# Kernel tuning notes

Hardware: AMD Instinct MI355X
Metric: run time of the kernel (lower is better)

Reference implementation:

```python
import jax, jax.numpy as jnp
import numpy as np
from jax.ops import segment_sum

N_GRAPHS, N_PER = 100, 1000
N = N_GRAPHS * N_PER
DEG = 32
E = N * DEG
RATIO = 0.8
K = int(np.ceil(RATIO * N_PER))  # 800, equal-size graphs -> fixed k
F_IN, F_MID, F_OUT = 128, 16, 256


def setup_inputs() -> dict:
    key = jax.random.key(0)
    ks = jax.random.split(key, 10)
    x = jax.random.normal(ks[0], (N, F_IN), dtype=jnp.float32)
    # intra-graph random edges
    epg = E // N_GRAPHS
    src_l = jax.random.randint(ks[1], (N_GRAPHS, epg), 0, N_PER)
    dst_l = jax.random.randint(ks[2], (N_GRAPHS, epg), 0, N_PER)
    offs = (jnp.arange(N_GRAPHS) * N_PER)[:, None]
    edge_index = jnp.stack([(src_l + offs).reshape(-1), (dst_l + offs).reshape(-1)]).astype(jnp.int32)
    batch = jnp.repeat(jnp.arange(N_GRAPHS, dtype=jnp.int32), N_PER)
    s = lambda fan: 1.0 / np.sqrt(fan)
    W1 = jax.random.normal(ks[3], (F_IN, F_MID), dtype=jnp.float32) * s(F_IN)
    b1 = jnp.zeros((F_MID,), dtype=jnp.float32)
    w_rel = jax.random.normal(ks[4], (F_MID, 1), dtype=jnp.float32) * s(F_MID)
    b_rel = jnp.zeros((1,), dtype=jnp.float32)
    w_root = jax.random.normal(ks[5], (F_MID, 1), dtype=jnp.float32) * s(F_MID)
    W2 = jax.random.normal(ks[6], (F_MID, F_OUT), dtype=jnp.float32) * s(F_MID)
    b2 = jnp.zeros((F_OUT,), dtype=jnp.float32)
    return {"x": x, "edge_index": edge_index, "batch": batch,
            "W1": W1, "b1": b1, "w_rel": w_rel, "b_rel": b_rel,
            "w_root": w_root, "W2": W2, "b2": b2}


def _gcn(x, src, dst, W, b, self_w, ew, n):
    # GCNConv with self-loops: D^{-1/2}(A+I)D^{-1/2} X W + b; masked variant
    deg = segment_sum(ew, dst, num_segments=n) + self_w
    dis = jnp.where(deg > 0, jax.lax.rsqrt(deg), 0.0)
    xw = x @ W
    coef = ew * dis[src] * dis[dst]                       # [E]
    agg = segment_sum(xw[src] * coef[:, None], dst, num_segments=n)
    agg = agg + xw * (self_w * dis * dis)[:, None]        # self-loop term
    return agg + b


def reference(x, edge_index, batch, W1, b1, w_rel, b_rel, w_root, W2, b2):
    src, dst = edge_index[0], edge_index[1]
    ones_n = jnp.ones((N,), dtype=x.dtype)
    ones_e = jnp.ones((src.shape[0],), dtype=x.dtype)
    # conv1 + relu
    h = jax.nn.relu(_gcn(x, src, dst, W1, b1, ones_n, ones_e, N))
    # SAGPooling score: GraphConv(16,1) -> tanh
    agg = segment_sum(h[src], dst, num_segments=N)
    score = jnp.tanh((agg @ w_rel + h @ w_root + b_rel)[:, 0])  # [N]
    # per-graph top-k (equal graph sizes -> fixed K), expressed as node mask
    sc2 = score.reshape(N_GRAPHS, N_PER)
    _, idx = jax.lax.top_k(sc2, K)
    mask = jnp.zeros((N_GRAPHS, N_PER), dtype=x.dtype)
    mask = mask.at[jnp.arange(N_GRAPHS)[:, None], idx].set(1.0).reshape(-1)  # [N]
    h = h * (score * mask)[:, None]                       # x[perm] * score[perm]
    em = mask[src] * mask[dst]                            # filter_adj as edge mask
    # conv2 + relu on surviving nodes only
    h2 = jax.nn.relu(_gcn(h, src, dst, W2, b2, mask, em, N)) * mask[:, None]
    # global mean pool over surviving nodes per graph
    sums = segment_sum(h2, batch, num_segments=N_GRAPHS)
    cnt = segment_sum(mask, batch, num_segments=N_GRAPHS)
    return sums / cnt[:, None]
```

## Files before the change

kernel.cpp:

```cpp
#include <hip/hip_runtime.h>
#include <math.h>

#define N_NODES 100000
#define NG 100
#define N_PER 1000
#define N_EDGES 3200000
#define EPG 32000
#define EPG4 8000
#define EPGP 35008
#define K_TOP 800
#define F_IN 128
#define F_MID 16
#define F_OUT 256
#define SENT 1000

typedef __attribute__((ext_vector_type(8))) short short8;
typedef __attribute__((ext_vector_type(4))) float floatx4;

__device__ __forceinline__ unsigned short f2bf(float x) {
    union { float f; unsigned int u; } c; c.f = x;
    unsigned int u = c.u;
    u = u + 0x7FFF + ((u >> 16) & 1);
    return (unsigned short)(u >> 16);
}
__device__ __forceinline__ void add4(float4& a, const float4 b) {
    a.x += b.x; a.y += b.y; a.z += b.z; a.w += b.w;
}
__device__ __forceinline__ int fidx4(int s, int l) {
    return s * 16 + ((4 * (l + ((s >> 1) & 3))) & 15);
}
__device__ __forceinline__ unsigned int fkey(float f) {
    unsigned int u = __float_as_uint(f);
    return (u & 0x80000000u) ? ~u : (u | 0x80000000u);
}

__global__ __launch_bounds__(1024) void k_front(const float* __restrict__ x,
    const float* __restrict__ W1, const int* __restrict__ ei,
    unsigned short* __restrict__ csr, int* __restrict__ cntG, int* __restrict__ rsG,
    float* __restrict__ dis1G, float* __restrict__ xw1)
{
    int b = blockIdx.x, t = threadIdx.x;
    if (b < NG) {
        __shared__ int cnts[N_PER];
        __shared__ int cur[N_PER];
        __shared__ int rs[N_PER];
        __shared__ int scan[1024];
        int g = b, ebase = g * EPG, nbase = g * N_PER;
        const int4* dst4 = (const int4*)(ei + N_EDGES + ebase);
        const int4* src4 = (const int4*)(ei + ebase);
        int4 dreg[8], sreg[8];
        int ni = 0;
        for (int i = t; i < EPG4; i += 1024) { dreg[ni] = dst4[i]; sreg[ni] = src4[i]; ni++; }
        if (t < N_PER) { cnts[t] = 0; cur[t] = 0; }
        __syncthreads();
        for (int i = 0; i < ni; i++) {
            atomicAdd(&cnts[dreg[i].x - nbase], 1);
            atomicAdd(&cnts[dreg[i].y - nbase], 1);
            atomicAdd(&cnts[dreg[i].z - nbase], 1);
            atomicAdd(&cnts[dreg[i].w - nbase], 1);
        }
        __syncthreads();
        int c = (t < N_PER) ? cnts[t] : 0;
        int c4 = (c + 3) & ~3;
        scan[t] = c4;
        __syncthreads();
        for (int dd = 1; dd < 1024; dd <<= 1) {
            int v = (t >= dd) ? scan[t - dd] : 0;
            __syncthreads();
            scan[t] += v;
            __syncthreads();
        }
        int exc = scan[t] - c4;
        unsigned short* cg = csr + (size_t)g * EPGP;
        if (t < N_PER) {
            rs[t] = exc; rsG[nbase + t] = exc; cntG[nbase + t] = c;
            dis1G[nbase + t] = rsqrtf((float)c + 1.0f);
            for (int q = c; q < c4; q++) cg[exc + q] = (unsigned short)SENT;
        }
        __syncthreads();
        for (int i = 0; i < ni; i++) {
            int dl, p;
            dl = dreg[i].x - nbase; p = rs[dl] + atomicAdd(&cur[dl], 1); cg[p] = (unsigned short)(sreg[i].x - nbase);
            dl = dreg[i].y - nbase; p = rs[dl] + atomicAdd(&cur[dl], 1); cg[p] = (unsigned short)(sreg[i].y - nbase);
            dl = dreg[i].z - nbase; p = rs[dl] + atomicAdd(&cur[dl], 1); cg[p] = (unsigned short)(sreg[i].z - nbase);
            dl = dreg[i].w - nbase; p = rs[dl] + atomicAdd(&cur[dl], 1); cg[p] = (unsigned short)(sreg[i].w - nbase);
        }
    } else {
        __shared__ float xs[64 * 132];
        __shared__ float wsm[F_IN * F_MID];
        long tile = b - NG;
        long n0 = tile * 64;
        int nmax = (int)((N_NODES - n0 < 64) ? (N_NODES - n0) : 64);
        const float* xp = x + n0 * F_IN;
        for (int i = t; i < nmax * F_IN; i += 1024) {
            int n = i >> 7, k = i & 127;
            xs[n * 132 + k] = xp[i];
        }
        for (int i = t; i < F_IN * F_MID; i += 1024) wsm[i] = W1[i];
        __syncthreads();
        int node = t >> 4, j = t & 15;
        if (node < nmax) {
            const float* xr = xs + node * 132;
            float acc = 0.f;
#pragma unroll 16
            for (int k = 0; k < F_IN; k++) acc += xr[k] * wsm[k * F_MID + j];
            xw1[(n0 + node) * F_MID + j] = acc;
        }
    }
}

__global__ __launch_bounds__(1024) void k_mega(const unsigned short* __restrict__ csr,
    const int* __restrict__ cntG, const int* __restrict__ rsG,
    const float* __restrict__ dis1G, const float* __restrict__ xw1,
    const float* __restrict__ b1, const float* __restrict__ w_rel,
    const float* __restrict__ b_rel, const float* __restrict__ w_root,
    const float* __restrict__ W2, const float* __restrict__ b2,
    float* __restrict__ out)
{
    __shared__ __align__(16) float feat[(N_PER + 1) * F_MID];
    __shared__ __align__(16) unsigned short fbf[N_PER * F_MID];
    __shared__ __align__(16) unsigned short w2t[F_OUT * F_MID];
    __shared__ float sc[N_PER];
    __shared__ float msk[N_PER + 1];
    __shared__ float wsrc[N_PER + 1];
    __shared__ float hw[N_PER + 1];
    __shared__ float hro[N_PER];
    __shared__ float dis2a[N_PER];
    __shared__ float dis1l[N_PER];
    __shared__ int cntl[N_PER];
    __shared__ int rsl[N_PER];
    __shared__ int hist[1024];
    __shared__ float partial[F_OUT];
    __shared__ int sh_b1, sh_r1, sh_b2, sh_r2, sh_len, sh_cntgt;
    __shared__ float sh_thr;

    int t = threadIdx.x, g = blockIdx.x;
    int nbase = g * N_PER;
    const unsigned short* cg = csr + (size_t)g * EPGP;
    int grp = t >> 2, l = t & 3;

    if (t < N_PER) { cntl[t] = cntG[nbase + t]; rsl[t] = rsG[nbase + t]; dis1l[t] = dis1G[nbase + t]; }
    if (t == 0) { sh_cntgt = 0; sh_len = 0; }
    for (int i = t; i < F_OUT * F_MID; i += 1024) {
        int f = i >> 4, jj = i & 15;
        w2t[i] = f2bf(W2[jj * F_OUT + f]);
    }
    __syncthreads();

    {
        const float4* xsrc = (const float4*)(xw1 + (size_t)nbase * F_MID);
        for (int i = t; i < N_PER * 4; i += 1024) {
            int n = i >> 2, q = i & 3;
            float4 v = xsrc[i];
            float d = dis1l[n];
            v.x *= d; v.y *= d; v.z *= d; v.w *= d;
            *(float4*)(feat + fidx4(n, q)) = v;
        }
        if (t < 4) { float4 z = {0.f, 0.f, 0.f, 0.f}; *(float4*)(feat + fidx4(SENT, t)) = z; }
    }
    __syncthreads();

    float4 b14 = *(const float4*)(b1 + 4 * l);
    float4 wr4 = *(const float4*)(w_rel + 4 * l);
    float4 wo4 = *(const float4*)(w_root + 4 * l);
    float brel = b_rel[0];

    float4 hreg[4];
#pragma unroll
    for (int rr = 0; rr < 4; rr++) {
        int n = grp + 256 * rr;
        if (n < N_PER) {
            int c4 = (cntl[n] + 3) & ~3;
            const unsigned short* cp = cg + rsl[n];
            float4 a0 = {0,0,0,0}, a1 = a0, a2 = a0, a3 = a0;
            for (int k = 0; k < c4; k += 4) {
                uint2 wv = *(const uint2*)(cp + k);
                int s0 = wv.x & 0xFFFF, s1 = wv.x >> 16, s2 = wv.y & 0xFFFF, s3 = wv.y >> 16;
                add4(a0, *(const float4*)(feat + fidx4(s0, l)));
                add4(a1, *(const float4*)(feat + fidx4(s1, l)));
                add4(a2, *(const float4*)(feat + fidx4(s2, l)));
                add4(a3, *(const float4*)(feat + fidx4(s3, l)));
            }
            add4(a0, a1); add4(a2, a3); add4(a0, a2);
            float4 sf = *(const float4*)(feat + fidx4(n, l));
            float di = dis1l[n];
            float4 hv;
            hv.x = fmaxf(fmaf(di, a0.x + sf.x, b14.x), 0.f);
            hv.y = fmaxf(fmaf(di, a0.y + sf.y, b14.y), 0.f);
            hv.z = fmaxf(fmaf(di, a0.z + sf.z, b14.z), 0.f);
            hv.w = fmaxf(fmaf(di, a0.w + sf.w, b14.w), 0.f);
            hreg[rr] = hv;
        }
    }
    __syncthreads();
#pragma unroll
    for (int rr = 0; rr < 4; rr++) {
        int n = grp + 256 * rr;
        if (n < N_PER) *(float4*)(feat + fidx4(n, l)) = hreg[rr];
    }
    __syncthreads();

#pragma unroll
    for (int rr = 0; rr < 4; rr++) {
        int n = grp + 256 * rr;
        if (n < N_PER) {
            float4 hv = *(const float4*)(feat + fidx4(n, l));
            float p1 = hv.x * wr4.x + hv.y * wr4.y + hv.z * wr4.z + hv.w * wr4.w;
            float p2 = hv.x * wo4.x + hv.y * wo4.y + hv.z * wo4.z + hv.w * wo4.w;
            p1 += __shfl_xor(p1, 1); p1 += __shfl_xor(p1, 2);
            p2 += __shfl_xor(p2, 1); p2 += __shfl_xor(p2, 2);
            if (l == 0) { hw[n] = p1; hro[n] = p2; }
        }
    }
    if (t == 0) hw[SENT] = 0.f;
    __syncthreads();

#pragma unroll
    for (int rr = 0; rr < 4; rr++) {
        int n = grp + 256 * rr;
        if (n < N_PER) {
            int c4 = (cntl[n] + 3) & ~3;
            const unsigned short* cp = cg + rsl[n];
            float sm = 0.f;
            for (int k = 0; k < c4; k += 4) {
                uint2 wv = *(const uint2*)(cp + k);
                int s = (l == 0) ? (int)(wv.x & 0xFFFF) : (l == 1) ? (int)(wv.x >> 16)
                      : (l == 2) ? (int)(wv.y & 0xFFFF) : (int)(wv.y >> 16);
                sm += hw[s];
            }
            sm += __shfl_xor(sm, 1); sm += __shfl_xor(sm, 2);
            if (l == 0) sc[n] = tanhf(sm + hro[n] + brel);
        }
    }
    __syncthreads();

    unsigned int mykey = (t < N_PER) ? fkey(sc[t]) : 0u;
    hist[t] = 0;
    __syncthreads();
    if (t < N_PER) atomicAdd(&hist[mykey >> 22], 1);
    __syncthreads();
    {
        int v0 = hist[t]; __syncthreads();
        hist[1023 - t] = v0; __syncthreads();
        for (int dd = 1; dd < 1024; dd <<= 1) {
            int v = (t >= dd) ? hist[t - dd] : 0;
            __syncthreads(); hist[t] += v; __syncthreads();
        }
        int Sb = hist[1023 - t];
        int Snext = (t == 1023) ? 0 : hist[1022 - t];
        if (Sb >= K_TOP && Snext < K_TOP) { sh_b1 = t; sh_r1 = K_TOP - Snext; }
    }
    __syncthreads();
    int b1v = sh_b1, r1 = sh_r1;
    hist[t] = 0;
    __syncthreads();
    if (t < N_PER && (int)(mykey >> 22) == b1v) atomicAdd(&hist[(mykey >> 12) & 1023], 1);
    __syncthreads();
    {
        int v0 = hist[t]; __syncthreads();
        hist[1023 - t] = v0; __syncthreads();
        for (int dd = 1; dd < 1024; dd <<= 1) {
            int v = (t >= dd) ? hist[t - dd] : 0;
            __syncthreads(); hist[t] += v; __syncthreads();
        }
        int Sb = hist[1023 - t];
        int Snext = (t == 1023) ? 0 : hist[1022 - t];
        if (Sb >= r1 && Snext < r1) { sh_b2 = t; sh_r2 = r1 - Snext; }
    }
    __syncthreads();
    unsigned int pref = ((unsigned int)b1v << 10) | (unsigned int)sh_b2;
    int r2 = sh_r2;
    __syncthreads();
    if (t < N_PER && (mykey >> 12) == pref) { int p = atomicAdd(&sh_len, 1); hist[p] = (int)mykey; }
    __syncthreads();
    {
        int L = sh_len;
        if (t < L) {
            unsigned int k0 = (unsigned int)hist[t];
            int gcnt = 0, ecnt = 0;
            for (int q2 = 0; q2 < L; q2++) {
                unsigned int kq = (unsigned int)hist[q2];
                gcnt += (kq > k0); ecnt += (kq == k0);
            }
            if (gcnt < r2 && r2 <= gcnt + ecnt)
                sh_thr = __uint_as_float((k0 & 0x80000000u) ? (k0 & 0x7FFFFFFFu) : ~k0);
        }
    }
    __syncthreads();
    float thr = sh_thr;

    {
        bool pred = (t < N_PER) && (sc[t] > thr);
        unsigned long long bal = __ballot(pred);
        if ((t & 63) == 0) atomicAdd(&sh_cntgt, (int)__popcll(bal));
    }
    __syncthreads();
    {
        int need = K_TOP - sh_cntgt;
        if (t < N_PER) {
            float v = sc[t];
            float mm;
            if (v > thr) mm = 1.f;
            else if (v < thr) mm = 0.f;
            else {
                int r = 0;
                for (int q2 = 0; q2 < t; q2++) if (sc[q2] == thr) r++;
                mm = (r < need) ? 1.f : 0.f;
            }
            msk[t] = mm;
        }
        if (t == 0) { msk[SENT] = 0.f; wsrc[SENT] = 0.f; }
    }
    __syncthreads();

#pragma unroll
    for (int rr = 0; rr < 4; rr++) {
        int n = grp + 256 * rr;
        if (n < N_PER) {
            int c4 = (cntl[n] + 3) & ~3;
            const unsigned short* cp = cg + rsl[n];
            float sm = 0.f;
            for (int k = 0; k < c4; k += 4) {
                uint2 wv = *(const uint2*)(cp + k);
                int s = (l == 0) ? (int)(wv.x & 0xFFFF) : (l == 1) ? (int)(wv.x >> 16)
                      : (l == 2) ? (int)(wv.y & 0xFFFF) : (int)(wv.y >> 16);
                sm += msk[s];
            }
            sm += __shfl_xor(sm, 1); sm += __shfl_xor(sm, 2);
            if (l == 0) {
                float d2 = msk[n] * (sm + 1.f);
                float di = (d2 > 0.f) ? rsqrtf(d2) : 0.f;
                dis2a[n] = di;
                wsrc[n] = sc[n] * msk[n] * di;
            }
        }
    }
    __syncthreads();

    for (int i = t; i < N_PER * 4; i += 1024) {
        int n = i >> 2, q = i & 3;
        float w = wsrc[n];
        float4* p = (float4*)(feat + fidx4(n, q));
        float4 v = *p;
        v.x *= w; v.y *= w; v.z *= w; v.w *= w;
        *p = v;
    }
    __syncthreads();

    float4 preg[4];
#pragma unroll
    for (int rr = 0; rr < 4; rr++) {
        int n = grp + 256 * rr;
        if (n < N_PER) {
            float di = dis2a[n];
            float4 pv = {0,0,0,0};
            if (di != 0.f) {
                int c4 = (cntl[n] + 3) & ~3;
                const unsigned short* cp = cg + rsl[n];
                float4 a0 = {0,0,0,0}, a1 = a0, a2 = a0, a3 = a0;
                for (int k = 0; k < c4; k += 4) {
                    uint2 wv = *(const uint2*)(cp + k);
                    int s0 = wv.x & 0xFFFF, s1 = wv.x >> 16, s2 = wv.y & 0xFFFF, s3 = wv.y >> 16;
                    add4(a0, *(const float4*)(feat + fidx4(s0, l)));
                    add4(a1, *(const float4*)(feat + fidx4(s1, l)));
                    add4(a2, *(const float4*)(feat + fidx4(s2, l)));
                    add4(a3, *(const float4*)(feat + fidx4(s3, l)));
                }
                add4(a0, a1); add4(a2, a3); add4(a0, a2);
                float4 sf = *(const float4*)(feat + fidx4(n, l));
                pv.x = di * (a0.x + sf.x);
                pv.y = di * (a0.y + sf.y);
                pv.z = di * (a0.z + sf.z);
                pv.w = di * (a0.w + sf.w);
            }
            preg[rr] = pv;
        }
    }
    __syncthreads();
#pragma unroll
    for (int rr = 0; rr < 4; rr++) {
        int n = grp + 256 * rr;
        if (n < N_PER) *(float4*)(feat + fidx4(n, l)) = preg[rr];
    }
    __syncthreads();

    for (int i = t; i < N_PER * 8; i += 1024) {
        int n = i >> 3, cp2 = (i & 7) * 2;
        int phys = n * 16 + ((cp2 + 4 * ((n >> 1) & 3)) & 15);
        float2 v = *(const float2*)(feat + phys);
        unsigned int pk = (unsigned int)f2bf(v.x) | ((unsigned int)f2bf(v.y) << 16);
        ((unsigned int*)fbf)[i] = pk;
    }
    __syncthreads();

    {
        int wave = t >> 6, lane = t & 63;
        int q = lane >> 4, fl = lane & 15;
        int half = wave >> 3, wcol = wave & 7;
        int c0 = 32 * wcol + fl, c1 = c0 + 16;
        float b2f0 = b2[c0], b2f1 = b2[c1];
        short8 bfrag0 = {0,0,0,0,0,0,0,0}, bfrag1 = bfrag0;
        if (q < 2) {
            bfrag0 = *(const short8*)(w2t + c0 * F_MID + q * 8);
            bfrag1 = *(const short8*)(w2t + c1 * F_MID + q * 8);
        }
        floatx4 zero = {0.f, 0.f, 0.f, 0.f};
        float acc0 = 0.f, acc1 = 0.f;
        int t0 = half ? 32 : 0, t1 = half ? 63 : 32;
        for (int tile = t0; tile < t1; tile++) {
            short8 afrag = {0,0,0,0,0,0,0,0};
            int na = tile * 16 + fl;
            if (q < 2 && na < N_PER)
                afrag = *(const short8*)(fbf + na * F_MID + q * 8);
            floatx4 d0 = __builtin_amdgcn_mfma_f32_16x16x32_bf16(afrag, bfrag0, zero, 0, 0, 0);
            floatx4 d1 = __builtin_amdgcn_mfma_f32_16x16x32_bf16(afrag, bfrag1, zero, 0, 0, 0);
#pragma unroll
            for (int r = 0; r < 4; r++) {
                int nd = tile * 16 + q * 4 + r;
                if (nd < N_PER) {
                    float m = msk[nd];
                    acc0 += m * fmaxf(d0[r] + b2f0, 0.f);
                    acc1 += m * fmaxf(d1[r] + b2f1, 0.f);
                }
            }
        }
        acc0 += __shfl_xor(acc0, 16); acc0 += __shfl_xor(acc0, 32);
        acc1 += __shfl_xor(acc1, 16); acc1 += __shfl_xor(acc1, 32);
        if (half == 0 && lane < 16) { partial[c0] = acc0; partial[c1] = acc1; }
        __syncthreads();
        if (half == 1 && lane < 16) {
            out[g * F_OUT + c0] = (partial[c0] + acc0) * (1.0f / (float)K_TOP);
            out[g * F_OUT + c1] = (partial[c1] + acc1) * (1.0f / (float)K_TOP);
        }
    }
}

extern "C" void kernel_launch(void* const* d_in, const int* in_sizes, int n_in,
                              void* d_out, int out_size, void* d_ws, size_t ws_size,
                              hipStream_t stream) {
    const float* x      = (const float*)d_in[0];
    const int*   ei     = (const int*)d_in[1];
    const float* W1     = (const float*)d_in[3];
    const float* b1     = (const float*)d_in[4];
    const float* w_rel  = (const float*)d_in[5];
    const float* b_rel  = (const float*)d_in[6];
    const float* w_root = (const float*)d_in[7];
    const float* W2     = (const float*)d_in[8];
    const float* b2     = (const float*)d_in[9];
    float* out = (float*)d_out;

    char* ws = (char*)d_ws;
    size_t o = 0;
    unsigned short* csr = (unsigned short*)(ws + o); o += (size_t)NG * EPGP * sizeof(unsigned short);
    int*   cntG  = (int*)(ws + o);   o += (size_t)N_NODES * sizeof(int);
    int*   rsG   = (int*)(ws + o);   o += (size_t)N_NODES * sizeof(int);
    float* dis1G = (float*)(ws + o); o += (size_t)N_NODES * sizeof(float);
    float* xw1   = (float*)(ws + o); o += (size_t)N_NODES * F_MID * sizeof(float);

    int gemm_blocks = (N_NODES + 63) / 64;
    k_front<<<NG + gemm_blocks, 1024, 0, stream>>>(x, W1, ei, csr, cntG, rsG, dis1G, xw1);
    k_mega<<<NG, 1024, 0, stream>>>(csr, cntG, rsG, dis1G, xw1,
                                    b1, w_rel, b_rel, w_root, W2, b2, out);
}
```

Measured before the change: 240.7 us.

## Use split-bf16 MFMA for first GEMM, pad CSR to 8, simplify top-k selection

Replaces the scalar x@W1 GEMM with a three-term split-bf16 MFMA (hi*hi + lo*hi + hi*lo) over 256-row tiles, and merges shared memory across the two roles of the front kernel. CSR rows are padded to multiples of 8 so the gathers load eight indices at a time into eight accumulators. The two-level radix top-k becomes one histogram level with wave-shuffle scans plus direct candidate ranking, and tie ranking uses bitmasks instead of a linear scan. Costs include more sentinel padding and memory, a single-level selection that may leave a large candidate bucket to rank, and slightly different GEMM rounding.

Result: no change. 241.8 us (+0.4%).

```diff
diff --git a/kernel.cpp b/kernel.cpp
--- a/kernel.cpp
+++ b/kernel.cpp
@@ -7,12 +7,14 @@
 #define N_EDGES 3200000
 #define EPG 32000
 #define EPG4 8000
-#define EPGP 35008
+#define EPGP 39008
 #define K_TOP 800
 #define F_IN 128
 #define F_MID 16
 #define F_OUT 256
 #define SENT 1000
+#define GEMM_ROWS 256
+#define GEMM_BLOCKS ((N_NODES + GEMM_ROWS - 1) / GEMM_ROWS)
 
 typedef __attribute__((ext_vector_type(8))) short short8;
 typedef __attribute__((ext_vector_type(4))) float floatx4;
@@ -23,6 +25,9 @@
     u = u + 0x7FFF + ((u >> 16) & 1);
     return (unsigned short)(u >> 16);
 }
+__device__ __forceinline__ float bf2f(unsigned short h) {
+    return __uint_as_float(((unsigned int)h) << 16);
+}
 __device__ __forceinline__ void add4(float4& a, const float4 b) {
     a.x += b.x; a.y += b.y; a.z += b.z; a.w += b.w;
 }
@@ -33,36 +38,38 @@
     unsigned int u = __float_as_uint(f);
     return (u & 0x80000000u) ? ~u : (u | 0x80000000u);
 }
+__device__ __forceinline__ float unfkey(unsigned int k) {
+    return __uint_as_float((k & 0x80000000u) ? (k & 0x7FFFFFFFu) : ~k);
+}
 
 __global__ __launch_bounds__(1024) void k_front(const float* __restrict__ x,
     const float* __restrict__ W1, const int* __restrict__ ei,
-    unsigned short* __restrict__ csr, int* __restrict__ cntG, int* __restrict__ rsG,
+    unsigned short* __restrict__ csr, int* __restrict__ cnt8G, int* __restrict__ rsG,
     float* __restrict__ dis1G, float* __restrict__ xw1)
 {
+    __shared__ __align__(16) char smem[16640];
     int b = blockIdx.x, t = threadIdx.x;
     if (b < NG) {
-        __shared__ int cnts[N_PER];
-        __shared__ int cur[N_PER];
-        __shared__ int rs[N_PER];
-        __shared__ int scan[1024];
+        int* cnts = (int*)smem;
+        int* cur  = (int*)(smem + 4000);
+        int* rs   = (int*)(smem + 8000);
+        int* scan = (int*)(smem + 12000);
         int g = b, ebase = g * EPG, nbase = g * N_PER;
         const int4* dst4 = (const int4*)(ei + N_EDGES + ebase);
         const int4* src4 = (const int4*)(ei + ebase);
-        int4 dreg[8], sreg[8];
-        int ni = 0;
-        for (int i = t; i < EPG4; i += 1024) { dreg[ni] = dst4[i]; sreg[ni] = src4[i]; ni++; }
         if (t < N_PER) { cnts[t] = 0; cur[t] = 0; }
         __syncthreads();
-        for (int i = 0; i < ni; i++) {
-            atomicAdd(&cnts[dreg[i].x - nbase], 1);
-            atomicAdd(&cnts[dreg[i].y - nbase], 1);
-            atomicAdd(&cnts[dreg[i].z - nbase], 1);
-            atomicAdd(&cnts[dreg[i].w - nbase], 1);
+        for (int i = t; i < EPG4; i += 1024) {
+            int4 d = dst4[i];
+            atomicAdd(&cnts[d.x - nbase], 1);
+            atomicAdd(&cnts[d.y - nbase], 1);
+            atomicAdd(&cnts[d.z - nbase], 1);
+            atomicAdd(&cnts[d.w - nbase], 1);
         }
         __syncthreads();
         int c = (t < N_PER) ? cnts[t] : 0;
-        int c4 = (c + 3) & ~3;
-        scan[t] = c4;
+        int c8 = (c + 7) & ~7;
+        scan[t] = c8;
         __syncthreads();
         for (int dd = 1; dd < 1024; dd <<= 1) {
             int v = (t >= dd) ? scan[t - dd] : 0;
@@ -70,47 +77,72 @@
             scan[t] += v;
             __syncthreads();
         }
-        int exc = scan[t] - c4;
+        int exc = scan[t] - c8;
         unsigned short* cg = csr + (size_t)g * EPGP;
         if (t < N_PER) {
-            rs[t] = exc; rsG[nbase + t] = exc; cntG[nbase + t] = c;
+            rs[t] = exc; rsG[nbase + t] = exc; cnt8G[nbase + t] = c8;
             dis1G[nbase + t] = rsqrtf((float)c + 1.0f);
-            for (int q = c; q < c4; q++) cg[exc + q] = (unsigned short)SENT;
-        }
-        __syncthreads();
-        for (int i = 0; i < ni; i++) {
+            for (int q = c; q < c8; q++) cg[exc + q] = (unsigned short)SENT;
+        }
+        __syncthreads();
+        for (int i = t; i < EPG4; i += 1024) {
+            int4 s4 = src4[i]; int4 d4 = dst4[i];
             int dl, p;
-            dl = dreg[i].x - nbase; p = rs[dl] + atomicAdd(&cur[dl], 1); cg[p] = (unsigned short)(sreg[i].x - nbase);
-            dl = dreg[i].y - nbase; p = rs[dl] + atomicAdd(&cur[dl], 1); cg[p] = (unsigned short)(sreg[i].y - nbase);
-            dl = dreg[i].z - nbase; p = rs[dl] + atomicAdd(&cur[dl], 1); cg[p] = (unsigned short)(sreg[i].z - nbase);
-            dl = dreg[i].w - nbase; p = rs[dl] + atomicAdd(&cur[dl], 1); cg[p] = (unsigned short)(sreg[i].w - nbase);
+            dl = d4.x - nbase; p = rs[dl] + atomicAdd(&cur[dl], 1); cg[p] = (unsigned short)(s4.x - nbase);
+            dl = d4.y - nbase; p = rs[dl] + atomicAdd(&cur[dl], 1); cg[p] = (unsigned short)(s4.y - nbase);
+            dl = d4.z - nbase; p = rs[dl] + atomicAdd(&cur[dl], 1); cg[p] = (unsigned short)(s4.z - nbase);
+            dl = d4.w - nbase; p = rs[dl] + atomicAdd(&cur[dl], 1); cg[p] = (unsigned short)(s4.w - nbase);
         }
     } else {
-        __shared__ float xs[64 * 132];
-        __shared__ float wsm[F_IN * F_MID];
-        long tile = b - NG;
-        long n0 = tile * 64;
-        int nmax = (int)((N_NODES - n0 < 64) ? (N_NODES - n0) : 64);
-        const float* xp = x + n0 * F_IN;
-        for (int i = t; i < nmax * F_IN; i += 1024) {
-            int n = i >> 7, k = i & 127;
-            xs[n * 132 + k] = xp[i];
-        }
-        for (int i = t; i < F_IN * F_MID; i += 1024) wsm[i] = W1[i];
-        __syncthreads();
-        int node = t >> 4, j = t & 15;
-        if (node < nmax) {
-            const float* xr = xs + node * 132;
-            float acc = 0.f;
-#pragma unroll 16
-            for (int k = 0; k < F_IN; k++) acc += xr[k] * wsm[k * F_MID + j];
-            xw1[(n0 + node) * F_MID + j] = acc;
+        unsigned short* bTh = (unsigned short*)smem;
+        unsigned short* bTl = (unsigned short*)(smem + 4096);
+        for (int i = t; i < F_IN * F_MID; i += 1024) {
+            int k = i >> 4, n = i & 15;
+            float w = W1[i];
+            unsigned short hh = f2bf(w);
+            bTh[n * 128 + k] = hh;
+            bTl[n * 128 + k] = f2bf(w - bf2f(hh));
+        }
+        __syncthreads();
+        int wave = t >> 6, lane = t & 63;
+        int m = lane & 15, q = lane >> 4;
+        long rbase = (long)(b - NG) * GEMM_ROWS + wave * 16;
+        long arow = rbase + m;
+        const float* xr = x + ((arow < N_NODES) ? arow : (N_NODES - 1)) * F_IN;
+        short8 ah[4], al[4], bh[4], bl[4];
+#pragma unroll
+        for (int c = 0; c < 4; c++) {
+            float4 v0 = *(const float4*)(xr + 32 * c + 8 * q);
+            float4 v1 = *(const float4*)(xr + 32 * c + 8 * q + 4);
+            float vv[8] = {v0.x, v0.y, v0.z, v0.w, v1.x, v1.y, v1.z, v1.w};
+            short8 h8, l8;
+#pragma unroll
+            for (int i = 0; i < 8; i++) {
+                unsigned short hh = f2bf(vv[i]);
+                h8[i] = (short)hh;
+                l8[i] = (short)f2bf(vv[i] - bf2f(hh));
+            }
+            ah[c] = h8; al[c] = l8;
+            bh[c] = *(const short8*)(bTh + m * 128 + 32 * c + 8 * q);
+            bl[c] = *(const short8*)(bTl + m * 128 + 32 * c + 8 * q);
+        }
+        floatx4 acc = {0.f, 0.f, 0.f, 0.f};
+#pragma unroll
+        for (int c = 0; c < 4; c++) {
+            acc = __builtin_amdgcn_mfma_f32_16x16x32_bf16(ah[c], bh[c], acc, 0, 0, 0);
+            acc = __builtin_amdgcn_mfma_f32_16x16x32_bf16(al[c], bh[c], acc, 0, 0, 0);
+            acc = __builtin_amdgcn_mfma_f32_16x16x32_bf16(ah[c], bl[c], acc, 0, 0, 0);
+        }
+#pragma unroll
+        for (int r = 0; r < 4; r++) {
+            long orow = rbase + q * 4 + r;
+            if (orow < N_NODES) xw1[orow * F_MID + m] = acc[r];
         }
     }
 }
 
 __global__ __launch_bounds__(1024) void k_mega(const unsigned short* __restrict__ csr,
-    const int* __restrict__ cntG, const int* __restrict__ rsG,
+    const int* __restrict__ cnt8G, const int* __restrict__ rsG,
     const float* __restrict__ dis1G, const float* __restrict__ xw1,
     const float* __restrict__ b1, const float* __restrict__ w_rel,
     const float* __restrict__ b_rel, const float* __restrict__ w_root,
@@ -127,20 +159,24 @@
     __shared__ float hro[N_PER];
     __shared__ float dis2a[N_PER];
     __shared__ float dis1l[N_PER];
-    __shared__ int cntl[N_PER];
+    __shared__ int cnt8l[N_PER];
     __shared__ int rsl[N_PER];
     __shared__ int hist[1024];
     __shared__ float partial[F_OUT];
-    __shared__ int sh_b1, sh_r1, sh_b2, sh_r2, sh_len, sh_cntgt;
+    __shared__ int wtot[16], wexc[16];
+    __shared__ unsigned int tiebits[32];
+    __shared__ int sh_b1, sh_r1, sh_len, sh_cntgt;
     __shared__ float sh_thr;
 
     int t = threadIdx.x, g = blockIdx.x;
     int nbase = g * N_PER;
     const unsigned short* cg = csr + (size_t)g * EPGP;
     int grp = t >> 2, l = t & 3;
-
-    if (t < N_PER) { cntl[t] = cntG[nbase + t]; rsl[t] = rsG[nbase + t]; dis1l[t] = dis1G[nbase + t]; }
+    int lane = t & 63, wid = t >> 6;
+
+    if (t < N_PER) { cnt8l[t] = cnt8G[nbase + t]; rsl[t] = rsG[nbase + t]; dis1l[t] = dis1G[nbase + t]; }
     if (t == 0) { sh_cntgt = 0; sh_len = 0; }
+    if (t < 32) tiebits[t] = 0;
     for (int i = t; i < F_OUT * F_MID; i += 1024) {
         int f = i >> 4, jj = i & 15;
         w2t[i] = f2bf(W2[jj * F_OUT + f]);
@@ -170,25 +206,29 @@
     for (int rr = 0; rr < 4; rr++) {
         int n = grp + 256 * rr;
         if (n < N_PER) {
-            int c4 = (cntl[n] + 3) & ~3;
+            int c8 = cnt8l[n];
             const unsigned short* cp = cg + rsl[n];
-            float4 a0 = {0,0,0,0}, a1 = a0, a2 = a0, a3 = a0;
-            for (int k = 0; k < c4; k += 4) {
-                uint2 wv = *(const uint2*)(cp + k);
-                int s0 = wv.x & 0xFFFF, s1 = wv.x >> 16, s2 = wv.y & 0xFFFF, s3 = wv.y >> 16;
-                add4(a0, *(const float4*)(feat + fidx4(s0, l)));
-                add4(a1, *(const float4*)(feat + fidx4(s1, l)));
-                add4(a2, *(const float4*)(feat + fidx4(s2, l)));
-                add4(a3, *(const float4*)(feat + fidx4(s3, l)));
-            }
-            add4(a0, a1); add4(a2, a3); add4(a0, a2);
+            float4 A0 = {0,0,0,0}, A1 = A0, A2 = A0, A3 = A0, A4 = A0, A5 = A0, A6 = A0, A7 = A0;
+            for (int k = 0; k < c8; k += 8) {
+                uint4 wv = *(const uint4*)(cp + k);
+                add4(A0, *(const float4*)(feat + fidx4((int)(wv.x & 0xFFFF), l)));
+                add4(A1, *(const float4*)(feat + fidx4((int)(wv.x >> 16), l)));
+                add4(A2, *(const float4*)(feat + fidx4((int)(wv.y & 0xFFFF), l)));
+                add4(A3, *(const float4*)(feat + fidx4((int)(wv.y >> 16), l)));
+                add4(A4, *(const float4*)(feat + fidx4((int)(wv.z & 0xFFFF), l)));
+                add4(A5, *(const float4*)(feat + fidx4((int)(wv.z >> 16), l)));
+                add4(A6, *(const float4*)(feat + fidx4((int)(wv.w & 0xFFFF), l)));
+                add4(A7, *(const float4*)(feat + fidx4((int)(wv.w >> 16), l)));
+            }
+            add4(A0, A1); add4(A2, A3); add4(A4, A5); add4(A6, A7);
+            add4(A0, A2); add4(A4, A6); add4(A0, A4);
             float4 sf = *(const float4*)(feat + fidx4(n, l));
             float di = dis1l[n];
             float4 hv;
-            hv.x = fmaxf(fmaf(di, a0.x + sf.x, b14.x), 0.f);
-            hv.y = fmaxf(fmaf(di, a0.y + sf.y, b14.y), 0.f);
-            hv.z = fmaxf(fmaf(di, a0.z + sf.z, b14.z), 0.f);
-            hv.w = fmaxf(fmaf(di, a0.w + sf.w, b14.w), 0.f);
+            hv.x = fmaxf(fmaf(di, A0.x + sf.x, b14.x), 0.f);
+            hv.y = fmaxf(fmaf(di, A0.y + sf.y, b14.y), 0.f);
+            hv.z = fmaxf(fmaf(di, A0.z + sf.z, b14.z), 0.f);
+            hv.w = fmaxf(fmaf(di, A0.w + sf.w, b14.w), 0.f);
             hreg[rr] = hv;
         }
     }
@@ -219,62 +259,57 @@
     for (int rr = 0; rr < 4; rr++) {
         int n = grp + 256 * rr;
         if (n < N_PER) {
-            int c4 = (cntl[n] + 3) & ~3;
+            int c8 = cnt8l[n];
             const unsigned short* cp = cg + rsl[n];
-            float sm = 0.f;
-            for (int k = 0; k < c4; k += 4) {
-                uint2 wv = *(const uint2*)(cp + k);
-                int s = (l == 0) ? (int)(wv.x & 0xFFFF) : (l == 1) ? (int)(wv.x >> 16)
-                      : (l == 2) ? (int)(wv.y & 0xFFFF) : (int)(wv.y >> 16);
-                sm += hw[s];
-            }
+            float s0 = 0.f, s1 = 0.f;
+            for (int k = 0; k < c8; k += 8) {
+                uint4 wv = *(const uint4*)(cp + k);
+                int sa = (l == 0) ? (int)(wv.x & 0xFFFF) : (l == 1) ? (int)(wv.x >> 16)
+                       : (l == 2) ? (int)(wv.y & 0xFFFF) : (int)(wv.y >> 16);
+                int sb = (l == 0) ? (int)(wv.z & 0xFFFF) : (l == 1) ? (int)(wv.z >> 16)
+                       : (l == 2) ? (int)(wv.w & 0xFFFF) : (int)(wv.w >> 16);
+                s0 += hw[sa]; s1 += hw[sb];
+            }
+            float sm = s0 + s1;
             sm += __shfl_xor(sm, 1); sm += __shfl_xor(sm, 2);
             if (l == 0) sc[n] = tanhf(sm + hro[n] + brel);
         }
     }
     __syncthreads();
 
-    unsigned int mykey = (t < N_PER) ? fkey(sc[t]) : 0u;
+    unsigned int mykey = 0; int myb = -1;
+    if (t < N_PER) { mykey = fkey(sc[t]); myb = (int)(mykey >> 22); }
     hist[t] = 0;
     __syncthreads();
-    if (t < N_PER) atomicAdd(&hist[mykey >> 22], 1);
+    if (t < N_PER) atomicAdd(&hist[myb], 1);
     __syncthreads();
     {
-        int v0 = hist[t]; __syncthreads();
-        hist[1023 - t] = v0; __syncthreads();
-        for (int dd = 1; dd < 1024; dd <<= 1) {
-            int v = (t >= dd) ? hist[t - dd] : 0;
-            __syncthreads(); hist[t] += v; __syncthreads();
-        }
-        int Sb = hist[1023 - t];
-        int Snext = (t == 1023) ? 0 : hist[1022 - t];
-        if (Sb >= K_TOP && Snext < K_TOP) { sh_b1 = t; sh_r1 = K_TOP - Snext; }
-    }
-    __syncthreads();
-    int b1v = sh_b1, r1 = sh_r1;
-    hist[t] = 0;
-    __syncthreads();
-    if (t < N_PER && (int)(mykey >> 22) == b1v) atomicAdd(&hist[(mykey >> 12) & 1023], 1);
+        int cntb = hist[t];
+        int v = cntb;
+        for (int off = 1; off < 64; off <<= 1) {
+            int u = __shfl_down(v, off, 64);
+            if (lane + off < 64) v += u;
+        }
+        if (lane == 0) wtot[wid] = v;
+        __syncthreads();
+        if (wid == 0) {
+            int wv2 = (lane < 16) ? wtot[lane] : 0;
+            int sv = wv2;
+            for (int off = 1; off < 16; off <<= 1) {
+                int u = __shfl_down(sv, off, 64);
+                if (lane + off < 64) sv += u;
+            }
+            if (lane < 16) wexc[lane] = sv - wv2;
+        }
+        __syncthreads();
+        int S = v + wexc[wid];
+        if (S >= K_TOP && S - cntb < K_TOP) { sh_b1 = t; sh_r1 = K_TOP - (S - cntb); }
+    }
+    __syncthreads();
+    if (t < N_PER && myb == sh_b1) { int p = atomicAdd(&sh_len, 1); hist[p] = (int)mykey; }
     __syncthreads();
     {
-        int v0 = hist[t]; __syncthreads();
-        hist[1023 - t] = v0; __syncthreads();
-        for (int dd = 1; dd < 1024; dd <<= 1) {
-            int v = (t >= dd) ? hist[t - dd] : 0;
-            __syncthreads(); hist[t] += v; __syncthreads();
-        }
-        int Sb = hist[1023 - t];
-        int Snext = (t == 1023) ? 0 : hist[1022 - t];
-        if (Sb >= r1 && Snext < r1) { sh_b2 = t; sh_r2 = r1 - Snext; }
-    }
-    __syncthreads();
-    unsigned int pref = ((unsigned int)b1v << 10) | (unsigned int)sh_b2;
-    int r2 = sh_r2;
-    __syncthreads();
-    if (t < N_PER && (mykey >> 12) == pref) { int p = atomicAdd(&sh_len, 1); hist[p] = (int)mykey; }
-    __syncthreads();
-    {
-        int L = sh_len;
+        int L = sh_len, r1 = sh_r1;
         if (t < L) {
             unsigned int k0 = (unsigned int)hist[t];
             int gcnt = 0, ecnt = 0;
@@ -282,8 +317,7 @@
                 unsigned int kq = (unsigned int)hist[q2];
                 gcnt += (kq > k0); ecnt += (kq == k0);
             }
-            if (gcnt < r2 && r2 <= gcnt + ecnt)
-                sh_thr = __uint_as_float((k0 & 0x80000000u) ? (k0 & 0x7FFFFFFFu) : ~k0);
+            if (gcnt < r1 && r1 <= gcnt + ecnt) sh_thr = unfkey(k0);
         }
     }
     __syncthreads();
@@ -291,11 +325,11 @@
 
     {
         bool pred = (t < N_PER) && (sc[t] > thr);
+        bool tied = (t < N_PER) && (sc[t] == thr);
         unsigned long long bal = __ballot(pred);
         if ((t & 63) == 0) atomicAdd(&sh_cntgt, (int)__popcll(bal));
-    }
-    __syncthreads();
-    {
+        if (tied) atomicOr(&tiebits[t >> 5], 1u << (t & 31));
+        __syncthreads();
         int need = K_TOP - sh_cntgt;
         if (t < N_PER) {
             float v = sc[t];
@@ -303,9 +337,10 @@
             if (v > thr) mm = 1.f;
             else if (v < thr) mm = 0.f;
             else {
-                int r = 0;
-                for (int q2 = 0; q2 < t; q2++) if (sc[q2] == thr) r++;
-                mm = (r < need) ? 1.f : 0.f;
+                int w = t >> 5;
+                int rank = __popc(tiebits[w] & ((1u << (t & 31)) - 1u));
+                for (int ww = 0; ww < w; ww++) rank += __popc(tiebits[ww]);
+                mm = (rank < need) ? 1.f : 0.f;
             }
             msk[t] = mm;
         }
@@ -317,15 +352,18 @@
     for (int rr = 0; rr < 4; rr++) {
         int n = grp + 256 * rr;
         if (n < N_PER) {
-            int c4 = (cntl[n] + 3) & ~3;
+            int c8 = cnt8l[n];
             const unsigned short* cp = cg + rsl[n];
-            float sm = 0.f;
-            for (int k = 0; k < c4; k += 4) {
-                uint2 wv = *(const uint2*)(cp + k);
-                int s = (l == 0) ? (int)(wv.x & 0xFFFF) : (l == 1) ? (int)(wv.x >> 16)
-                      : (l == 2) ? (int)(wv.y & 0xFFFF) : (int)(wv.y >> 16);
-                sm += msk[s];
-            }
+            float s0 = 0.f, s1 = 0.f;
+            for (int k = 0; k < c8; k += 8) {
+                uint4 wv = *(const uint4*)(cp + k);
+                int sa = (l == 0) ? (int)(wv.x & 0xFFFF) : (l == 1) ? (int)(wv.x >> 16)
+                       : (l == 2) ? (int)(wv.y & 0xFFFF) : (int)(wv.y >> 16);
+                int sb = (l == 0) ? (int)(wv.z & 0xFFFF) : (l == 1) ? (int)(wv.z >> 16)
+                       : (l == 2) ? (int)(wv.w & 0xFFFF) : (int)(wv.w >> 16);
+                s0 += msk[sa]; s1 += msk[sb];
+            }
+            float sm = s0 + s1;
             sm += __shfl_xor(sm, 1); sm += __shfl_xor(sm, 2);
             if (l == 0) {
                 float d2 = msk[n] * (sm + 1.f);
@@ -355,23 +393,27 @@
             float di = dis2a[n];
             float4 pv = {0,0,0,0};
             if (di != 0.f) {
-                int c4 = (cntl[n] + 3) & ~3;
+                int c8 = cnt8l[n];
                 const unsigned short* cp = cg + rsl[n];
-                float4 a0 = {0,0,0,0}, a1 = a0, a2 = a0, a3 = a0;
-                for (int k = 0; k < c4; k += 4) {
-                    uint2 wv = *(const uint2*)(cp + k);
-                    int s0 = wv.x & 0xFFFF, s1 = wv.x >> 16, s2 = wv.y & 0xFFFF, s3 = wv.y >> 16;
-                    add4(a0, *(const float4*)(feat + fidx4(s0, l)));
-                    add4(a1, *(const float4*)(feat + fidx4(s1, l)));
-                    add4(a2, *(const float4*)(feat + fidx4(s2, l)));
-                    add4(a3, *(const float4*)(feat + fidx4(s3, l)));
+                float4 A0 = {0,0,0,0}, A1 = A0, A2 = A0, A3 = A0, A4 = A0, A5 = A0, A6 = A0, A7 = A0;
+                for (int k = 0; k < c8; k += 8) {
+                    uint4 wv = *(const uint4*)(cp + k);
+                    add4(A0, *(const float4*)(feat + fidx4((int)(wv.x & 0xFFFF), l)));
+                    add4(A1, *(const float4*)(feat + fidx4((int)(wv.x >> 16), l)));
+                    add4(A2, *(const float4*)(feat + fidx4((int)(wv.y & 0xFFFF), l)));
+                    add4(A3, *(const float4*)(feat + fidx4((int)(wv.y >> 16), l)));
+                    add4(A4, *(const float4*)(feat + fidx4((int)(wv.z & 0xFFFF), l)));
+                    add4(A5, *(const float4*)(feat + fidx4((int)(wv.z >> 16), l)));
+                    add4(A6, *(const float4*)(feat + fidx4((int)(wv.w & 0xFFFF), l)));
+                    add4(A7, *(const float4*)(feat + fidx4((int)(wv.w >> 16), l)));
                 }
-                add4(a0, a1); add4(a2, a3); add4(a0, a2);
+                add4(A0, A1); add4(A2, A3); add4(A4, A5); add4(A6, A7);
+                add4(A0, A2); add4(A4, A6); add4(A0, A4);
                 float4 sf = *(const float4*)(feat + fidx4(n, l));
-                pv.x = di * (a0.x + sf.x);
-                pv.y = di * (a0.y + sf.y);
-                pv.z = di * (a0.z + sf.z);
-                pv.w = di * (a0.w + sf.w);
+                pv.x = di * (A0.x + sf.x);
+                pv.y = di * (A0.y + sf.y);
+                pv.z = di * (A0.z + sf.z);
+                pv.w = di * (A0.w + sf.w);
             }
             preg[rr] = pv;
         }
@@ -394,9 +436,8 @@
     __syncthreads();
 
     {
-        int wave = t >> 6, lane = t & 63;
         int q = lane >> 4, fl = lane & 15;
-        int half = wave >> 3, wcol = wave & 7;
+        int half = wid >> 3, wcol = wid & 7;
         int c0 = 32 * wcol + fl, c1 = c0 + 16;
         float b2f0 = b2[c0], b2f1 = b2[c1];
         short8 bfrag0 = {0,0,0,0,0,0,0,0}, bfrag1 = bfrag0;
@@ -452,13 +493,12 @@
     char* ws = (char*)d_ws;
     size_t o = 0;
     unsigned short* csr = (unsigned short*)(ws + o); o += (size_t)NG * EPGP * sizeof(unsigned short);
-    int*   cntG  = (int*)(ws + o);   o += (size_t)N_NODES * sizeof(int);
+    int*   cnt8G = (int*)(ws + o);   o += (size_t)N_NODES * sizeof(int);
     int*   rsG   = (int*)(ws + o);   o += (size_t)N_NODES * sizeof(int);
     float* dis1G = (float*)(ws + o); o += (size_t)N_NODES * sizeof(float);
     float* xw1   = (float*)(ws + o); o += (size_t)N_NODES * F_MID * sizeof(float);
 
-    int gemm_blocks = (N_NODES + 63) / 64;
-    k_front<<<NG + gemm_blocks, 1024, 0, stream>>>(x, W1, ei, csr, cntG, rsG, dis1G, xw1);
-    k_mega<<<NG, 1024, 0, stream>>>(csr, cntG, rsG, dis1G, xw1,
+    k_front<<<NG + GEMM_BLOCKS, 1024, 0, stream>>>(x, W1, ei, csr, cnt8G, rsG, dis1G, xw1);
+    k_mega<<<NG, 1024, 0, stream>>>(csr, cnt8G, rsG, dis1G, xw1,
                                     b1, w_rel, b_rel, w_root, W2, b2, out);
 }
```
